# Kernel tuning notes

Measured on AMD Instinct MI355X. Metric: run time of the kernel, lower is better.

## Reference

```python
import jax, jax.numpy as jnp
import numpy as np

START_IDX = 1  # Offsets.GO
END_IDX = 2    # Offsets.EOS
NEG_INF = -10000.0


def setup_inputs() -> dict:
    key = jax.random.key(0)
    k1, k2, k3 = jax.random.split(key, 3)
    B, T, N = 256, 1024, 128
    unary = jax.random.normal(k1, (B, T, N), dtype=jnp.float32)
    trans = jax.random.normal(k2, (1, N, N), dtype=jnp.float32) * 0.1
    lengths = jax.random.randint(k3, (B,), 1, T + 1)
    return {"unary": unary, "trans": trans, "lengths": lengths}


def _forward_alg(unary_btn, trans, lengths):
    """CRF log-partition. unary_btn: [B,T,N], trans: [1,N,N], lengths: [B] -> [B]."""
    B, T, N = unary_btn.shape
    tr = trans[0]  # [N(cur), N(prev)]
    unary_tbn = jnp.transpose(unary_btn, (1, 0, 2))  # batch_first -> [T,B,N]

    init_alphas = jnp.full((B, N), NEG_INF, dtype=unary_btn.dtype)
    init_alphas = init_alphas.at[:, START_IDX].set(0.0)

    def step(alphas, inp):
        unary_t, t = inp  # unary_t: [B,N]
        # scores[b, i, j] = alphas[b, j] + trans[i, j] + unary_t[b, i]
        scores = alphas[:, None, :] + tr[None, :, :] + unary_t[:, :, None]
        new_alphas = jax.nn.logsumexp(scores, axis=2)  # [B,N]
        # only advance positions still inside the sequence
        alphas = jnp.where((t < lengths)[:, None], new_alphas, alphas)
        return alphas, None

    alphas, _ = jax.lax.scan(step, init_alphas, (unary_tbn, jnp.arange(T)))
    terminal = alphas + tr[END_IDX][None, :]  # trans[:, end_idx] row: [N]
    return jax.nn.logsumexp(terminal, axis=1)  # [B]


def reference(unary, trans, lengths):
    return _forward_alg(unary, trans, lengths)
```

## Files before the change

kernel.cpp:

```cpp
#include <hip/hip_runtime.h>

#define T_LEN 1024
#define NS    128
#define BT    16
#define G     16
#define SEG   64
#define SSH   6
#define NB    256

typedef __attribute__((ext_vector_type(8))) short short8;
typedef __attribute__((ext_vector_type(4))) short short4v;
typedef __attribute__((ext_vector_type(4))) float f32x4;

static __device__ __forceinline__ short f2bf(float f) {
    unsigned u = __builtin_bit_cast(unsigned, f);
    u = (u + 0x7fffu + ((u >> 16) & 1u)) >> 16;
    return (short)u;
}
static __device__ __forceinline__ float bf2f(short s) {
    unsigned u = ((unsigned)(unsigned short)s) << 16;
    return __builtin_bit_cast(float, u);
}
static __device__ __forceinline__ short f2bf_trunc(float f) {
    return (short)(__builtin_bit_cast(unsigned, f) >> 16);
}

__global__ __launch_bounds__(64, 2) void crf_seg(
        const float* __restrict__ unary, const float* __restrict__ trans,
        const int* __restrict__ lengths,
        float* __restrict__ yv, float* __restrict__ zv,
        float* __restrict__ cfv, float* __restrict__ cbv) {
    __shared__ __align__(16) short Fs[BT * NS];

    const int tid = threadIdx.x;
    const int g = blockIdx.x & (G - 1);
    const int u = blockIdx.x >> 4;
    const bool bwd = u >= (SEG - 1);
    const int s = bwd ? (u - (SEG - 2)) : u;
    const int quad = tid >> 4, bcol = tid & 15;

    const int Lb = lengths[g * BT + bcol];
    const int tb = (s * Lb) >> SSH, te = ((s + 1) * Lb) >> SSH;
    const int nrec = te - tb - 1;
    int dlen = te - tb;
    #pragma unroll
    for (int m = 1; m < 16; m <<= 1) {
        int o = __shfl_xor(dlen, m, 64);
        dlen = o > dlen ? o : dlen;
    }
    const int iters = dlen;

    short8 Ea[8][4];
    #pragma unroll
    for (int j = 0; j < 8; ++j) {
        const int i = j * 16 + bcol;
        #pragma unroll
        for (int kt = 0; kt < 4; ++kt) {
            short8 e;
            if (!bwd) {
                const float* tr = trans + (size_t)i * NS + kt * 32 + quad * 8;
                float4 x = *(const float4*)tr, y = *(const float4*)(tr + 4);
                e[0] = f2bf(__expf(x.x)); e[1] = f2bf(__expf(x.y));
                e[2] = f2bf(__expf(x.z)); e[3] = f2bf(__expf(x.w));
                e[4] = f2bf(__expf(y.x)); e[5] = f2bf(__expf(y.y));
                e[6] = f2bf(__expf(y.z)); e[7] = f2bf(__expf(y.w));
            } else {
                #pragma unroll
                for (int jj = 0; jj < 8; ++jj)
                    e[jj] = f2bf(__expf(trans[(size_t)(kt * 32 + quad * 8 + jj) * NS + i]));
            }
            Ea[j][kt] = e;
        }
    }

    #pragma unroll
    for (int rep = 0; rep < 4; ++rep) {
        const int tv = rep * 64 + tid;
        const int sr = tv >> 4, sc = tv & 15;
        const int Ls = lengths[g * BT + sr];
        const int s_tb = (s * Ls) >> SSH, s_te = ((s + 1) * Ls) >> SSH;
        const float* ubase = unary + (size_t)(g * BT + sr) * T_LEN * NS + sc * 8;
        float v[8];
        if (!bwd) {
            #pragma unroll
            for (int k = 0; k < 8; ++k)
                v[k] = (s == 0) ? ((sc * 8 + k == 1) ? 1.f : 0.f) : 1.f;
        } else {
            int ti = s_te - 1; if (ti < 0) ti = 0;
            const float* up = ubase + (size_t)ti * NS;
            float4 ua = *(const float4*)up, ub4 = *(const float4*)(up + 4);
            float uu[8] = {ua.x, ua.y, ua.z, ua.w, ub4.x, ub4.y, ub4.z, ub4.w};
            #pragma unroll
            for (int k = 0; k < 8; ++k) {
                float vv = (s == SEG - 1) ? __expf(trans[2 * NS + sc * 8 + k]) : 1.f;
                v[k] = __expf(uu[k]) * vv;
            }
        }
        short8 z;
        #pragma unroll
        for (int k = 0; k < 8; ++k) z[k] = f2bf(v[k]);
        *(short8*)&Fs[sr * NS + ((sc ^ sr) << 3)] = z;

        if (s_te == s_tb) {
            if (!bwd) {
                float* yp = yv + ((size_t)s * NB + g * BT + sr) * NS + sc * 8;
                #pragma unroll
                for (int k = 0; k < 8; ++k)
                    yp[k] = (s == 0) ? ((sc * 8 + k == 1) ? 1.f : 0.f) : 1.f;
                if (sc == 0) cfv[s * NB + g * BT + sr] = 0.f;
            } else {
                float* zp = zv + ((size_t)(s - 1) * NB + g * BT + sr) * NS + sc * 8;
                #pragma unroll
                for (int k = 0; k < 8; ++k) zp[k] = 1.f;
                if (sc == 0) cbv[(s - 1) * NB + g * BT + sr] = 0.f;
            }
        }
    }

    const float* uptr = unary + (size_t)(g * BT + bcol) * T_LEN * NS + quad * 4;
    #define T_OFB(nn) ({ int _t = bwd ? (te - 2 - (nn)) : (tb + (nn)); \
                         _t = _t < 0 ? 0 : (_t > T_LEN - 1 ? T_LEN - 1 : _t); _t; })
    float4 U[8];
    {
        int t = T_OFB(0);
        #pragma unroll
        for (int j = 0; j < 8; ++j) U[j] = *(const float4*)(uptr + (size_t)t * NS + j * 16);
    }

    int bfOff[4];
    #pragma unroll
    for (int kt = 0; kt < 4; ++kt) bfOff[kt] = bcol * NS + (((kt * 4 + quad) ^ bcol) << 3);
    const int s4Off = bcol * NS + (bcol << 3);
    int fwo[8];
    #pragma unroll
    for (int j = 0; j < 8; ++j) {
        const int cj = 2 * j + (quad >> 1);
        fwo[j] = bcol * NS + ((cj ^ bcol) << 3) + ((quad & 1) << 2);
    }

    asm volatile("s_waitcnt lgkmcnt(0)" ::: "memory");
    float C = 0.f;

    for (int n = 0; n < iters; ++n) {
        short8 Bf0 = *(const short8*)&Fs[bfOff[0]];
        short8 Bf1 = *(const short8*)&Fs[bfOff[1]];
        short8 Bf2 = *(const short8*)&Fs[bfOff[2]];
        short8 Bf3 = *(const short8*)&Fs[bfOff[3]];
        short4v s4 = *(const short4v*)&Fs[s4Off];

        float sv = (bf2f(s4[0]) + bf2f(s4[1])) + (bf2f(s4[2]) + bf2f(s4[3]));
        float rs = __fdividef(1.f, sv);
        float logs = __logf(sv);

        f32x4 acc[8];
        #pragma unroll
        for (int j = 0; j < 8; ++j) acc[j] = (f32x4){0.f, 0.f, 0.f, 0.f};
        #pragma unroll
        for (int j = 0; j < 8; ++j) acc[j] = __builtin_amdgcn_mfma_f32_16x16x32_bf16(Ea[j][0], Bf0, acc[j], 0, 0, 0);
        #pragma unroll
        for (int j = 0; j < 8; ++j) acc[j] = __builtin_amdgcn_mfma_f32_16x16x32_bf16(Ea[j][1], Bf1, acc[j], 0, 0, 0);
        #pragma unroll
        for (int j = 0; j < 8; ++j) acc[j] = __builtin_amdgcn_mfma_f32_16x16x32_bf16(Ea[j][2], Bf2, acc[j], 0, 0, 0);
        #pragma unroll
        for (int j = 0; j < 8; ++j) acc[j] = __builtin_amdgcn_mfma_f32_16x16x32_bf16(Ea[j][3], Bf3, acc[j], 0, 0, 0);

        if (bwd && n == nrec) {
            float* zp = zv + ((size_t)(s - 1) * NB + g * BT + bcol) * NS;
            #pragma unroll
            for (int j = 0; j < 8; ++j)
                *(float4*)(zp + j * 16 + quad * 4) = (float4){acc[j][0], acc[j][1], acc[j][2], acc[j][3]};
            if (tid < BT) cbv[(s - 1) * NB + g * BT + tid] = C;
        }

        {
            int t = T_OFB(n + 1);
            #pragma unroll
            for (int j = 0; j < 8; ++j) {
                float e0 = __expf(U[j].x), e1 = __expf(U[j].y);
                float e2 = __expf(U[j].z), e3 = __expf(U[j].w);
                acc[j][0] *= e0 * rs; acc[j][1] *= e1 * rs;
                acc[j][2] *= e2 * rs; acc[j][3] *= e3 * rs;
                U[j] = *(const float4*)(uptr + (size_t)t * NS + j * 16);
            }
        }

        if (!bwd && n == nrec) {
            float* yp = yv + ((size_t)s * NB + g * BT + bcol) * NS;
            #pragma unroll
            for (int j = 0; j < 8; ++j)
                *(float4*)(yp + j * 16 + quad * 4) = (float4){acc[j][0], acc[j][1], acc[j][2], acc[j][3]};
            if (tid < BT) cfv[s * NB + g * BT + tid] = C + logs;
        }
        C += logs;

        #pragma unroll
        for (int j = 0; j < 8; ++j) {
            short4v p;
            p[0] = f2bf_trunc(acc[j][0]); p[1] = f2bf_trunc(acc[j][1]);
            p[2] = f2bf_trunc(acc[j][2]); p[3] = f2bf_trunc(acc[j][3]);
            *(short4v*)&Fs[fwo[j]] = p;
        }
        asm volatile("s_waitcnt lgkmcnt(0)" ::: "memory");
    }
#undef T_OFB
}

__global__ __launch_bounds__(256) void crf_combine(
        const float* __restrict__ yv, const float* __restrict__ zv,
        const float* __restrict__ cfv, const float* __restrict__ cbv,
        float* __restrict__ out) {
    __shared__ float part[4];
    const int b = blockIdx.x, tid = threadIdx.x;
    const int w = tid >> 6, lane = tid & 63;
    float lg = 0.f;
    for (int s = 1 + w; s <= SEG - 1; s += 4) lg += cbv[(s - 1) * NB + b];
    for (int s = 1 + w; s <= SEG - 1; s += 4) {
        const float* Z = zv + ((size_t)(s - 1) * NB + b) * NS;
        const float* Y = yv + ((size_t)(s - 1) * NB + b) * NS;
        float d = Z[lane] * Y[lane] + Z[lane + 64] * Y[lane + 64];
        #pragma unroll
        for (int off = 1; off < 64; off <<= 1) d += __shfl_xor(d, off, 64);
        lg += __logf(d);
    }
    for (int s = 1 + w; s <= SEG - 2; s += 4) {
        const float* Y = yv + ((size_t)s * NB + b) * NS;
        float t = Y[lane] + Y[lane + 64];
        #pragma unroll
        for (int off = 1; off < 64; off <<= 1) t += __shfl_xor(t, off, 64);
        lg -= __logf(t);
    }
    if (lane == 0) part[w] = lg;
    __syncthreads();
    if (tid == 0) out[b] = cfv[b] + ((part[0] + part[1]) + (part[2] + part[3]));
}

extern "C" void kernel_launch(void* const* d_in, const int* in_sizes, int n_in,
                              void* d_out, int out_size, void* d_ws, size_t ws_size,
                              hipStream_t stream) {
    const float* unary   = (const float*)d_in[0];
    const float* trans   = (const float*)d_in[1];
    const int*   lengths = (const int*)d_in[2];
    float* out = (float*)d_out;

    float* yv  = (float*)d_ws;
    float* zv  = yv + (size_t)(SEG - 1) * NB * NS;
    float* cfv = zv + (size_t)(SEG - 1) * NB * NS;
    float* cbv = cfv + (size_t)(SEG - 1) * NB;

    crf_seg<<<dim3(2 * (SEG - 1) * G), dim3(64), 0, stream>>>(
        unary, trans, lengths, yv, zv, cfv, cbv);
    crf_combine<<<dim3(NB), dim3(256), 0, stream>>>(yv, zv, cfv, cbv, out);
}
```

Baseline: 245.6 us.

## Fuse forward and backward segment passes, caching exp(unary) in LDS

Each block now handles one segment and runs both directions: the forward recurrence stores bf16 exp(unary) values in shared memory, and the backward recurrence reuses them instead of re-reading unary from global memory. Segment count doubles to 128 while block count stays the same, so each segment is half as long. The forward loop is unrolled by two with double-buffered prefetch of unary rows. The cost is a larger LDS footprint (ST=8 steps), occupancy lowered to one wave per SIMD in launch bounds, and twice the serial steps per block. The backward pass also reads the bf16-rounded exponentials rather than fp32 values.

```diff
diff --git a/kernel.cpp b/kernel.cpp
--- a/kernel.cpp
+++ b/kernel.cpp
@@ -4,8 +4,9 @@
 #define NS    128
 #define BT    16
 #define G     16
-#define SEG   64
-#define SSH   6
+#define SEG   128
+#define SSH   7
+#define ST    8
 #define NB    256
 
 typedef __attribute__((ext_vector_type(8))) short short8;
@@ -25,24 +26,24 @@
     return (short)(__builtin_bit_cast(unsigned, f) >> 16);
 }
 
-__global__ __launch_bounds__(64, 2) void crf_seg(
+__global__ __launch_bounds__(64, 1) void crf_seg(
         const float* __restrict__ unary, const float* __restrict__ trans,
         const int* __restrict__ lengths,
         float* __restrict__ yv, float* __restrict__ zv,
         float* __restrict__ cfv, float* __restrict__ cbv) {
     __shared__ __align__(16) short Fs[BT * NS];
+    __shared__ __align__(16) short EU[ST * BT * NS];
 
     const int tid = threadIdx.x;
     const int g = blockIdx.x & (G - 1);
-    const int u = blockIdx.x >> 4;
-    const bool bwd = u >= (SEG - 1);
-    const int s = bwd ? (u - (SEG - 2)) : u;
+    const int s = blockIdx.x >> 4;
     const int quad = tid >> 4, bcol = tid & 15;
 
     const int Lb = lengths[g * BT + bcol];
     const int tb = (s * Lb) >> SSH, te = ((s + 1) * Lb) >> SSH;
-    const int nrec = te - tb - 1;
-    int dlen = te - tb;
+    const int slen = te - tb;
+    const int nrec = slen - 1;
+    int dlen = slen;
     #pragma unroll
     for (int m = 1; m < 16; m <<= 1) {
         int o = __shfl_xor(dlen, m, 64);
@@ -56,19 +57,13 @@
         const int i = j * 16 + bcol;
         #pragma unroll
         for (int kt = 0; kt < 4; ++kt) {
+            const float* tr = trans + (size_t)i * NS + kt * 32 + quad * 8;
+            float4 x = *(const float4*)tr, y = *(const float4*)(tr + 4);
             short8 e;
-            if (!bwd) {
-                const float* tr = trans + (size_t)i * NS + kt * 32 + quad * 8;
-                float4 x = *(const float4*)tr, y = *(const float4*)(tr + 4);
-                e[0] = f2bf(__expf(x.x)); e[1] = f2bf(__expf(x.y));
-                e[2] = f2bf(__expf(x.z)); e[3] = f2bf(__expf(x.w));
-                e[4] = f2bf(__expf(y.x)); e[5] = f2bf(__expf(y.y));
-                e[6] = f2bf(__expf(y.z)); e[7] = f2bf(__expf(y.w));
-            } else {
-                #pragma unroll
-                for (int jj = 0; jj < 8; ++jj)
-                    e[jj] = f2bf(__expf(trans[(size_t)(kt * 32 + quad * 8 + jj) * NS + i]));
-            }
+            e[0] = f2bf(__expf(x.x)); e[1] = f2bf(__expf(x.y));
+            e[2] = f2bf(__expf(x.z)); e[3] = f2bf(__expf(x.w));
+            e[4] = f2bf(__expf(y.x)); e[5] = f2bf(__expf(y.y));
+            e[6] = f2bf(__expf(y.z)); e[7] = f2bf(__expf(y.w));
             Ea[j][kt] = e;
         }
     }
@@ -79,130 +74,208 @@
         const int sr = tv >> 4, sc = tv & 15;
         const int Ls = lengths[g * BT + sr];
         const int s_tb = (s * Ls) >> SSH, s_te = ((s + 1) * Ls) >> SSH;
-        const float* ubase = unary + (size_t)(g * BT + sr) * T_LEN * NS + sc * 8;
         float v[8];
-        if (!bwd) {
+        #pragma unroll
+        for (int k = 0; k < 8; ++k)
+            v[k] = (s == 0) ? ((sc * 8 + k == 1) ? 1.f : 0.f) : 1.f;
+        short8 z;
+        #pragma unroll
+        for (int k = 0; k < 8; ++k) z[k] = f2bf(v[k]);
+        *(short8*)&Fs[sr * NS + ((sc ^ sr) << 3)] = z;
+
+        if (s_te == s_tb && s < SEG - 1) {
+            float* yp = yv + ((size_t)s * NB + g * BT + sr) * NS + sc * 8;
             #pragma unroll
             for (int k = 0; k < 8; ++k)
-                v[k] = (s == 0) ? ((sc * 8 + k == 1) ? 1.f : 0.f) : 1.f;
-        } else {
-            int ti = s_te - 1; if (ti < 0) ti = 0;
-            const float* up = ubase + (size_t)ti * NS;
-            float4 ua = *(const float4*)up, ub4 = *(const float4*)(up + 4);
-            float uu[8] = {ua.x, ua.y, ua.z, ua.w, ub4.x, ub4.y, ub4.z, ub4.w};
-            #pragma unroll
-            for (int k = 0; k < 8; ++k) {
-                float vv = (s == SEG - 1) ? __expf(trans[2 * NS + sc * 8 + k]) : 1.f;
-                v[k] = __expf(uu[k]) * vv;
-            }
-        }
-        short8 z;
-        #pragma unroll
-        for (int k = 0; k < 8; ++k) z[k] = f2bf(v[k]);
-        *(short8*)&Fs[sr * NS + ((sc ^ sr) << 3)] = z;
-
-        if (s_te == s_tb) {
-            if (!bwd) {
-                float* yp = yv + ((size_t)s * NB + g * BT + sr) * NS + sc * 8;
-                #pragma unroll
-                for (int k = 0; k < 8; ++k)
-                    yp[k] = (s == 0) ? ((sc * 8 + k == 1) ? 1.f : 0.f) : 1.f;
-                if (sc == 0) cfv[s * NB + g * BT + sr] = 0.f;
-            } else {
-                float* zp = zv + ((size_t)(s - 1) * NB + g * BT + sr) * NS + sc * 8;
-                #pragma unroll
-                for (int k = 0; k < 8; ++k) zp[k] = 1.f;
-                if (sc == 0) cbv[(s - 1) * NB + g * BT + sr] = 0.f;
-            }
+                yp[k] = (s == 0) ? ((sc * 8 + k == 1) ? 1.f : 0.f) : 1.f;
+            if (sc == 0) cfv[s * NB + g * BT + sr] = 0.f;
         }
     }
 
     const float* uptr = unary + (size_t)(g * BT + bcol) * T_LEN * NS + quad * 4;
-    #define T_OFB(nn) ({ int _t = bwd ? (te - 2 - (nn)) : (tb + (nn)); \
-                         _t = _t < 0 ? 0 : (_t > T_LEN - 1 ? T_LEN - 1 : _t); _t; })
-    float4 U[8];
+    const int slenc = slen > 0 ? slen - 1 : 0;
+    #define T_F(nn) (tb + ((nn) < slen ? (nn) : slenc))
+    float4 pA[8], pB[8];
     {
-        int t = T_OFB(0);
-        #pragma unroll
-        for (int j = 0; j < 8; ++j) U[j] = *(const float4*)(uptr + (size_t)t * NS + j * 16);
+        int t = T_F(0);
+        #pragma unroll
+        for (int j = 0; j < 8; ++j) pA[j] = *(const float4*)(uptr + (size_t)t * NS + j * 16);
+        t = T_F(1);
+        #pragma unroll
+        for (int j = 0; j < 8; ++j) pB[j] = *(const float4*)(uptr + (size_t)t * NS + j * 16);
     }
 
     int bfOff[4];
     #pragma unroll
     for (int kt = 0; kt < 4; ++kt) bfOff[kt] = bcol * NS + (((kt * 4 + quad) ^ bcol) << 3);
     const int s4Off = bcol * NS + (bcol << 3);
-    int fwo[8];
+    int fwo[8], euW[8];
     #pragma unroll
     for (int j = 0; j < 8; ++j) {
         const int cj = 2 * j + (quad >> 1);
         fwo[j] = bcol * NS + ((cj ^ bcol) << 3) + ((quad & 1) << 2);
+        euW[j] = bcol * NS + (((cj ^ bcol) & 15) << 3) + ((quad & 1) << 2);
     }
 
     asm volatile("s_waitcnt lgkmcnt(0)" ::: "memory");
     float C = 0.f;
 
-    for (int n = 0; n < iters; ++n) {
-        short8 Bf0 = *(const short8*)&Fs[bfOff[0]];
-        short8 Bf1 = *(const short8*)&Fs[bfOff[1]];
-        short8 Bf2 = *(const short8*)&Fs[bfOff[2]];
-        short8 Bf3 = *(const short8*)&Fs[bfOff[3]];
-        short4v s4 = *(const short4v*)&Fs[s4Off];
-
-        float sv = (bf2f(s4[0]) + bf2f(s4[1])) + (bf2f(s4[2]) + bf2f(s4[3]));
-        float rs = __fdividef(1.f, sv);
-        float logs = __logf(sv);
-
-        f32x4 acc[8];
-        #pragma unroll
-        for (int j = 0; j < 8; ++j) acc[j] = (f32x4){0.f, 0.f, 0.f, 0.f};
-        #pragma unroll
-        for (int j = 0; j < 8; ++j) acc[j] = __builtin_amdgcn_mfma_f32_16x16x32_bf16(Ea[j][0], Bf0, acc[j], 0, 0, 0);
-        #pragma unroll
-        for (int j = 0; j < 8; ++j) acc[j] = __builtin_amdgcn_mfma_f32_16x16x32_bf16(Ea[j][1], Bf1, acc[j], 0, 0, 0);
-        #pragma unroll
-        for (int j = 0; j < 8; ++j) acc[j] = __builtin_amdgcn_mfma_f32_16x16x32_bf16(Ea[j][2], Bf2, acc[j], 0, 0, 0);
-        #pragma unroll
-        for (int j = 0; j < 8; ++j) acc[j] = __builtin_amdgcn_mfma_f32_16x16x32_bf16(Ea[j][3], Bf3, acc[j], 0, 0, 0);
-
-        if (bwd && n == nrec) {
-            float* zp = zv + ((size_t)(s - 1) * NB + g * BT + bcol) * NS;
-            #pragma unroll
-            for (int j = 0; j < 8; ++j)
-                *(float4*)(zp + j * 16 + quad * 4) = (float4){acc[j][0], acc[j][1], acc[j][2], acc[j][3]};
-            if (tid < BT) cbv[(s - 1) * NB + g * BT + tid] = C;
-        }
-
-        {
-            int t = T_OFB(n + 1);
+#define STEP_F(U) do {                                                            \
+    short8 Bf0 = *(const short8*)&Fs[bfOff[0]];                                   \
+    short8 Bf1 = *(const short8*)&Fs[bfOff[1]];                                   \
+    short8 Bf2 = *(const short8*)&Fs[bfOff[2]];                                   \
+    short8 Bf3 = *(const short8*)&Fs[bfOff[3]];                                   \
+    short4v s4 = *(const short4v*)&Fs[s4Off];                                     \
+    float sv = (bf2f(s4[0]) + bf2f(s4[1])) + (bf2f(s4[2]) + bf2f(s4[3]));         \
+    float rs = __fdividef(1.f, sv);                                               \
+    float logs = __logf(sv);                                                      \
+    f32x4 acc[8];                                                                 \
+    _Pragma("unroll")                                                             \
+    for (int j = 0; j < 8; ++j) acc[j] = (f32x4){0.f, 0.f, 0.f, 0.f};             \
+    _Pragma("unroll")                                                             \
+    for (int j = 0; j < 8; ++j) acc[j] = __builtin_amdgcn_mfma_f32_16x16x32_bf16(Ea[j][0], Bf0, acc[j], 0, 0, 0); \
+    _Pragma("unroll")                                                             \
+    for (int j = 0; j < 8; ++j) acc[j] = __builtin_amdgcn_mfma_f32_16x16x32_bf16(Ea[j][1], Bf1, acc[j], 0, 0, 0); \
+    _Pragma("unroll")                                                             \
+    for (int j = 0; j < 8; ++j) acc[j] = __builtin_amdgcn_mfma_f32_16x16x32_bf16(Ea[j][2], Bf2, acc[j], 0, 0, 0); \
+    _Pragma("unroll")                                                             \
+    for (int j = 0; j < 8; ++j) acc[j] = __builtin_amdgcn_mfma_f32_16x16x32_bf16(Ea[j][3], Bf3, acc[j], 0, 0, 0); \
+    const int eub = n * (BT * NS);                                                \
+    int t2 = T_F(n + 2);                                                          \
+    _Pragma("unroll")                                                             \
+    for (int j = 0; j < 8; ++j) {                                                 \
+        float e0 = __expf(U[j].x), e1 = __expf(U[j].y);                           \
+        float e2 = __expf(U[j].z), e3 = __expf(U[j].w);                           \
+        short4v w;                                                                \
+        w[0] = f2bf(e0); w[1] = f2bf(e1); w[2] = f2bf(e2); w[3] = f2bf(e3);       \
+        *(short4v*)&EU[eub + euW[j]] = w;                                         \
+        acc[j][0] *= e0 * rs; acc[j][1] *= e1 * rs;                               \
+        acc[j][2] *= e2 * rs; acc[j][3] *= e3 * rs;                               \
+        U[j] = *(const float4*)(uptr + (size_t)t2 * NS + j * 16);                 \
+    }                                                                             \
+    if (s < SEG - 1 && n == nrec) {    \
+        float* yp = yv + ((size_t)s * NB + g * BT + bcol) * NS;                   \
+        _Pragma("unroll")                                                         \
+        for (int j = 0; j < 8; ++j)                                               \
+            *(float4*)(yp + j * 16 + quad * 4) = (float4){acc[j][0], acc[j][1], acc[j][2], acc[j][3]}; \
+        if (tid < BT) cfv[s * NB + g * BT + tid] = C + logs;                      \
+    }                                                                             \
+    C += logs;                                                                    \
+    _Pragma("unroll")                                                             \
+    for (int j = 0; j < 8; ++j) {                                                 \
+        short4v p;                                                                \
+        p[0] = f2bf_trunc(acc[j][0]); p[1] = f2bf_trunc(acc[j][1]);               \
+        p[2] = f2bf_trunc(acc[j][2]); p[3] = f2bf_trunc(acc[j][3]);               \
+        *(short4v*)&Fs[fwo[j]] = p;                                               \
+    }                                                                             \
+    asm volatile("s_waitcnt lgkmcnt(0)" ::: "memory");                            \
+} while (0)
+
+    for (int n = 0; n < iters; ) {
+        STEP_F(pA); ++n;
+        if (n >= iters) break;
+        STEP_F(pB); ++n;
+    }
+#undef STEP_F
+#undef T_F
+
+    if (s != 0) {
+        if (iters > 0) {
             #pragma unroll
             for (int j = 0; j < 8; ++j) {
-                float e0 = __expf(U[j].x), e1 = __expf(U[j].y);
-                float e2 = __expf(U[j].z), e3 = __expf(U[j].w);
-                acc[j][0] *= e0 * rs; acc[j][1] *= e1 * rs;
-                acc[j][2] *= e2 * rs; acc[j][3] *= e3 * rs;
-                U[j] = *(const float4*)(uptr + (size_t)t * NS + j * 16);
+                const int i = j * 16 + bcol;
+                #pragma unroll
+                for (int kt = 0; kt < 4; ++kt) {
+                    short8 e;
+                    #pragma unroll
+                    for (int jj = 0; jj < 8; ++jj)
+                        e[jj] = f2bf(__expf(trans[(size_t)(kt * 32 + quad * 8 + jj) * NS + i]));
+                    Ea[j][kt] = e;
+                }
             }
         }
-
-        if (!bwd && n == nrec) {
-            float* yp = yv + ((size_t)s * NB + g * BT + bcol) * NS;
-            #pragma unroll
-            for (int j = 0; j < 8; ++j)
-                *(float4*)(yp + j * 16 + quad * 4) = (float4){acc[j][0], acc[j][1], acc[j][2], acc[j][3]};
-            if (tid < BT) cfv[s * NB + g * BT + tid] = C + logs;
-        }
-        C += logs;
-
-        #pragma unroll
-        for (int j = 0; j < 8; ++j) {
-            short4v p;
-            p[0] = f2bf_trunc(acc[j][0]); p[1] = f2bf_trunc(acc[j][1]);
-            p[2] = f2bf_trunc(acc[j][2]); p[3] = f2bf_trunc(acc[j][3]);
-            *(short4v*)&Fs[fwo[j]] = p;
-        }
-        asm volatile("s_waitcnt lgkmcnt(0)" ::: "memory");
-    }
-#undef T_OFB
+        #pragma unroll
+        for (int rep = 0; rep < 4; ++rep) {
+            const int tv = rep * 64 + tid;
+            const int sr = tv >> 4, sc = tv & 15;
+            const int Ls = lengths[g * BT + sr];
+            const int s_tb = (s * Ls) >> SSH, s_te = ((s + 1) * Ls) >> SSH;
+            const int sl = s_te - s_tb;
+            if (sl == 0) {
+                float* zp = zv + ((size_t)(s - 1) * NB + g * BT + sr) * NS + sc * 8;
+                #pragma unroll
+                for (int k = 0; k < 8; ++k) zp[k] = 1.f;
+                if (sc == 0) cbv[(s - 1) * NB + g * BT + sr] = 0.f;
+                short8 z;
+                #pragma unroll
+                for (int k = 0; k < 8; ++k) z[k] = f2bf(1.f);
+                *(short8*)&Fs[sr * NS + ((sc ^ sr) << 3)] = z;
+            } else {
+                const int r0 = sl - 1;
+                short8 eu8 = *(const short8*)&EU[r0 * (BT * NS) + sr * NS + (((sc ^ sr) & 15) << 3)];
+                short8 z;
+                #pragma unroll
+                for (int k = 0; k < 8; ++k) {
+                    float vv = (s == SEG - 1) ? __expf(trans[2 * NS + sc * 8 + k]) : 1.f;
+                    z[k] = f2bf(bf2f(eu8[k]) * vv);
+                }
+                *(short8*)&Fs[sr * NS + ((sc ^ sr) << 3)] = z;
+            }
+        }
+
+        if (iters > 0) {
+            asm volatile("s_waitcnt lgkmcnt(0)" ::: "memory");
+            float Cb = 0.f;
+            for (int m = 0; m < iters; ++m) {
+                short8 Bf0 = *(const short8*)&Fs[bfOff[0]];
+                short8 Bf1 = *(const short8*)&Fs[bfOff[1]];
+                short8 Bf2 = *(const short8*)&Fs[bfOff[2]];
+                short8 Bf3 = *(const short8*)&Fs[bfOff[3]];
+                short4v s4 = *(const short4v*)&Fs[s4Off];
+                float sv = (bf2f(s4[0]) + bf2f(s4[1])) + (bf2f(s4[2]) + bf2f(s4[3]));
+                float rs = __fdividef(1.f, sv);
+                float logs = __logf(sv);
+                f32x4 acc[8];
+                #pragma unroll
+                for (int j = 0; j < 8; ++j) acc[j] = (f32x4){0.f, 0.f, 0.f, 0.f};
+                #pragma unroll
+                for (int j = 0; j < 8; ++j) acc[j] = __builtin_amdgcn_mfma_f32_16x16x32_bf16(Ea[j][0], Bf0, acc[j], 0, 0, 0);
+                #pragma unroll
+                for (int j = 0; j < 8; ++j) acc[j] = __builtin_amdgcn_mfma_f32_16x16x32_bf16(Ea[j][1], Bf1, acc[j], 0, 0, 0);
+                #pragma unroll
+                for (int j = 0; j < 8; ++j) acc[j] = __builtin_amdgcn_mfma_f32_16x16x32_bf16(Ea[j][2], Bf2, acc[j], 0, 0, 0);
+                #pragma unroll
+                for (int j = 0; j < 8; ++j) acc[j] = __builtin_amdgcn_mfma_f32_16x16x32_bf16(Ea[j][3], Bf3, acc[j], 0, 0, 0);
+
+                if (m == nrec) {
+                    float* zp = zv + ((size_t)(s - 1) * NB + g * BT + bcol) * NS;
+                    #pragma unroll
+                    for (int j = 0; j < 8; ++j)
+                        *(float4*)(zp + j * 16 + quad * 4) = (float4){acc[j][0], acc[j][1], acc[j][2], acc[j][3]};
+                    if (tid < BT) cbv[(s - 1) * NB + g * BT + tid] = Cb;
+                }
+
+                int r = slen - 2 - m; r = r < 0 ? 0 : r;
+                const int rb = r * (BT * NS);
+                #pragma unroll
+                for (int j = 0; j < 8; ++j) {
+                    short4v ev = *(const short4v*)&EU[rb + euW[j]];
+                    acc[j][0] *= bf2f(ev[0]) * rs; acc[j][1] *= bf2f(ev[1]) * rs;
+                    acc[j][2] *= bf2f(ev[2]) * rs; acc[j][3] *= bf2f(ev[3]) * rs;
+                }
+                Cb += logs;
+
+                #pragma unroll
+                for (int j = 0; j < 8; ++j) {
+                    short4v p;
+                    p[0] = f2bf_trunc(acc[j][0]); p[1] = f2bf_trunc(acc[j][1]);
+                    p[2] = f2bf_trunc(acc[j][2]); p[3] = f2bf_trunc(acc[j][3]);
+                    *(short4v*)&Fs[fwo[j]] = p;
+                }
+                asm volatile("s_waitcnt lgkmcnt(0)" ::: "memory");
+            }
+        }
+    }
 }
 
 __global__ __launch_bounds__(256) void crf_combine(
@@ -247,7 +320,7 @@
     float* cfv = zv + (size_t)(SEG - 1) * NB * NS;
     float* cbv = cfv + (size_t)(SEG - 1) * NB;
 
-    crf_seg<<<dim3(2 * (SEG - 1) * G), dim3(64), 0, stream>>>(
+    crf_seg<<<dim3(SEG * G), dim3(64), 0, stream>>>(
         unary, trans, lengths, yv, zv, cfv, cbv);
     crf_combine<<<dim3(NB), dim3(256), 0, stream>>>(yv, zv, cfv, cbv, out);
 }
```

Result: slower. 269.7 us (+9.8%).
